# Kernel tuning notes

Hardware: AMD Instinct MI355X
Metric: run time of the kernel (lower is better)

The kernel has to match this reference:

```python
import jax, jax.numpy as jnp
import numpy as np

N = 100000
E = 800000
IN_DIM = 256
HEADS = 8
OUT_DIM = 32
OUT_ALL = HEADS * OUT_DIM  # 256 == IN_DIM -> residual is Identity
NEG_SLOPE = 0.2


def setup_inputs() -> dict:
    key = jax.random.key(0)
    ks = jax.random.split(key, 10)
    s_in = 1.0 / np.sqrt(IN_DIM)
    x = jax.random.normal(ks[0], (N, IN_DIM), dtype=jnp.float32)
    edge_index = jax.random.randint(ks[1], (2, E), 0, N, dtype=jnp.int64)
    Wl = jax.random.normal(ks[2], (IN_DIM, OUT_ALL), dtype=jnp.float32) * s_in
    bl = jnp.zeros((OUT_ALL,), dtype=jnp.float32)
    Wr = jax.random.normal(ks[3], (IN_DIM, OUT_ALL), dtype=jnp.float32) * s_in
    br = jnp.zeros((OUT_ALL,), dtype=jnp.float32)
    att = jax.random.normal(ks[4], (HEADS, OUT_DIM), dtype=jnp.float32) * (1.0 / np.sqrt(OUT_DIM))
    bias = jnp.zeros((OUT_ALL,), dtype=jnp.float32)
    gamma = jnp.ones((OUT_ALL,), dtype=jnp.float32)
    beta = jnp.zeros((OUT_ALL,), dtype=jnp.float32)
    return {"x": x, "edge_index": edge_index, "Wl": Wl, "bl": bl, "Wr": Wr,
            "br": br, "att": att, "bias": bias, "gamma": gamma, "beta": beta}


def reference(x, edge_index, Wl, bl, Wr, br, att, bias, gamma, beta):
    src, dst = edge_index[0], edge_index[1]
    # GATv2: separate transforms for source (lin_l) and target (lin_r)
    x_l = (x @ Wl + bl).reshape(N, HEADS, OUT_DIM)  # messages / source side
    x_r = (x @ Wr + br).reshape(N, HEADS, OUT_DIM)  # target side
    # edge-wise GATv2 score: a^T LeakyReLU(x_j + x_i)
    s = jax.nn.leaky_relu(x_l[src] + x_r[dst], NEG_SLOPE)  # [E, H, D]
    e = jnp.einsum('ehd,hd->eh', s, att)                   # [E, H]
    # segment softmax over incoming edges of each destination node
    m = jax.ops.segment_max(e, dst, num_segments=N)        # [N, H]
    p = jnp.exp(e - m[dst])                                # [E, H]
    denom = jax.ops.segment_sum(p, dst, num_segments=N)    # [N, H]
    denom = jnp.where(denom == 0, 1.0, denom)
    alpha = p / denom[dst]                                 # [E, H]
    # scatter-sum aggregate of alpha * lin_l(x_src)
    msg = alpha[:, :, None] * x_l[src]                     # [E, H, D]
    out = jax.ops.segment_sum(msg, dst, num_segments=N)    # [N, H, D]
    y = out.reshape(N, OUT_ALL) + bias
    # residual is Identity since in_dim == heads*out_dim
    z = y + x
    # LayerNorm then ELU
    mu = jnp.mean(z, axis=-1, keepdims=True)
    var = jnp.var(z, axis=-1, keepdims=True)
    zn = (z - mu) * jax.lax.rsqrt(var + 1e-5) * gamma + beta
    return jax.nn.elu(zn)
```

## Files before the change

### kernel.cpp

```cpp
#include <hip/hip_runtime.h>
#include <hip/hip_bf16.h>

#define NN 100000
#define EE 800000
#define DALL 256
#define NEG 0.2f

#define CNT_BLOCKS 3125
#define CVTW_BLOCKS 128
#define CVTX_BLOCKS 2048

typedef __attribute__((ext_vector_type(8))) short bf16x8;
typedef __attribute__((ext_vector_type(4))) float f32x4;

static __device__ __forceinline__ ushort f2b(float f) {
    __hip_bfloat16 h = __float2bfloat16(f);
    return *reinterpret_cast<ushort*>(&h);
}
static __device__ __forceinline__ float b2f(ushort u) {
    union { float f; unsigned v; } c; c.v = ((unsigned)u) << 16; return c.f;
}
static __device__ __forceinline__ void unpack8(uint4 u, float* v) {
    v[0] = b2f((ushort)(u.x & 0xffff)); v[1] = b2f((ushort)(u.x >> 16));
    v[2] = b2f((ushort)(u.y & 0xffff)); v[3] = b2f((ushort)(u.y >> 16));
    v[4] = b2f((ushort)(u.z & 0xffff)); v[5] = b2f((ushort)(u.z >> 16));
    v[6] = b2f((ushort)(u.w & 0xffff)); v[7] = b2f((ushort)(u.w >> 16));
}

__global__ __launch_bounds__(256) void fused_init(
    const float* __restrict__ x, const float* __restrict__ Wl,
    const float* __restrict__ Wr, const int* __restrict__ dst,
    ushort* __restrict__ xb, ushort* __restrict__ Wt, int* __restrict__ cnt)
{
    __shared__ float tile[32][33];
    int b = blockIdx.x;
    if (b < CNT_BLOCKS) {
        int e = b * 256 + threadIdx.x;
        if (e < EE) atomicAdd(&cnt[dst[e]], 1);
        return;
    }
    b -= CNT_BLOCKS;
    if (b < CVTW_BLOCKS) {
        int kt = (b & 7) * 32, nt = (b >> 3) * 32;
        int tx = threadIdx.x & 31, ty = threadIdx.x >> 5;
#pragma unroll
        for (int i = 0; i < 32; i += 8) {
            int k = kt + ty + i, n = nt + tx;
            float v = (n < 256) ? Wl[(size_t)k * 256 + n] : Wr[(size_t)k * 256 + (n - 256)];
            tile[ty + i][tx] = v;
        }
        __syncthreads();
#pragma unroll
        for (int i = 0; i < 32; i += 8) {
            int n = nt + ty + i, k = kt + tx;
            Wt[(size_t)n * 256 + k] = f2b(tile[tx][ty + i]);
        }
        return;
    }
    b -= CVTW_BLOCKS;
    const int total = NN * DALL / 8;
    for (int i = b * 256 + threadIdx.x; i < total; i += CVTX_BLOCKS * 256) {
        float4 a = reinterpret_cast<const float4*>(x)[i * 2];
        float4 c = reinterpret_cast<const float4*>(x)[i * 2 + 1];
        uint4 o;
        o.x = f2b(a.x) | ((unsigned)f2b(a.y) << 16);
        o.y = f2b(a.z) | ((unsigned)f2b(a.w) << 16);
        o.z = f2b(c.x) | ((unsigned)f2b(c.y) << 16);
        o.w = f2b(c.z) | ((unsigned)f2b(c.w) << 16);
        reinterpret_cast<uint4*>(xb)[i] = o;
    }
}

__global__ __launch_bounds__(512) void gemm_dual(
    const ushort* __restrict__ xb,
    const ushort* __restrict__ Wt,
    const float* __restrict__ bl, const float* __restrict__ br,
    ushort* __restrict__ xl, ushort* __restrict__ xr)
{
    __shared__ __align__(16) ushort smemA[2][128 * 32];
    __shared__ __align__(16) ushort smemB[2][256 * 32];

    const int bx = blockIdx.x;
    const int rowBase = (bx >> 1) * 128;
    const int colBase = (bx & 1) * 256;
    const int t = threadIdx.x, lane = t & 63, wave = t >> 6;
    const int wr = (wave >> 2) * 64;
    const int wc = (wave & 3) * 64;

    f32x4 acc[4][4];
#pragma unroll
    for (int m = 0; m < 4; ++m)
#pragma unroll
        for (int n = 0; n < 4; ++n) acc[m][n] = (f32x4){0.f, 0.f, 0.f, 0.f};

    auto STAGE = [&](int buf, int kb) {
        {
            int rc = t >> 2, slot = t & 3;
            int ga = rowBase + rc; if (ga >= NN) ga = NN - 1;
            const ushort* gp = xb + (size_t)ga * 256 + kb + slot * 8;
            ushort* lp = &smemA[buf][wave * 512];
            __builtin_amdgcn_global_load_lds(
                (const __attribute__((address_space(1))) unsigned int*)gp,
                (__attribute__((address_space(3))) unsigned int*)lp, 16, 0, 0);
        }
#pragma unroll
        for (int i = 0; i < 2; ++i) {
            int c = i * 512 + t;
            int rc = c >> 2, slot = c & 3;
            const ushort* gp = Wt + (size_t)(colBase + rc) * 256 + kb + slot * 8;
            ushort* lp = &smemB[buf][(i * 512 + wave * 64) * 8];
            __builtin_amdgcn_global_load_lds(
                (const __attribute__((address_space(1))) unsigned int*)gp,
                (__attribute__((address_space(3))) unsigned int*)lp, 16, 0, 0);
        }
    };

    STAGE(0, 0);
    __syncthreads();

#pragma unroll
    for (int s = 0; s < 8; ++s) {
        if (s < 7) STAGE((s + 1) & 1, (s + 1) * 32);
        const ushort* A = smemA[s & 1];
        const ushort* B = smemB[s & 1];
        bf16x8 af[4], bfr[4];
#pragma unroll
        for (int m = 0; m < 4; ++m)
            af[m] = *reinterpret_cast<const bf16x8*>(
                &A[(wr + m * 16 + (lane & 15)) * 32 + (lane >> 4) * 8]);
#pragma unroll
        for (int n = 0; n < 4; ++n)
            bfr[n] = *reinterpret_cast<const bf16x8*>(
                &B[(wc + n * 16 + (lane & 15)) * 32 + (lane >> 4) * 8]);
#pragma unroll
        for (int m = 0; m < 4; ++m)
#pragma unroll
            for (int n = 0; n < 4; ++n)
                acc[m][n] = __builtin_amdgcn_mfma_f32_16x16x32_bf16(
                    af[m], bfr[n], acc[m][n], 0, 0, 0);
        if (s < 7) __syncthreads();
    }

    const bool isL = (colBase == 0);
    ushort* OutP = isL ? xl : xr;
    const float* bvp = isL ? bl : br;

    int colLoc[4]; float bb[4];
#pragma unroll
    for (int n = 0; n < 4; ++n) {
        colLoc[n] = wc + n * 16 + (lane & 15);
        bb[n] = bvp[colLoc[n]];
    }
#pragma unroll
    for (int m = 0; m < 4; ++m) {
        int r0 = rowBase + wr + m * 16 + (lane >> 4) * 4;
#pragma unroll
        for (int r = 0; r < 4; ++r) {
            int row = r0 + r;
            if (row < NN) {
#pragma unroll
                for (int n = 0; n < 4; ++n)
                    OutP[(size_t)row * 256 + colLoc[n]] = f2b(acc[m][n][r] + bb[n]);
            }
        }
    }
}

__global__ __launch_bounds__(256) void scan_part1(const int* __restrict__ cnt,
                                                  int* __restrict__ bsums)
{
    __shared__ int red[256];
    int base = blockIdx.x * 1024 + threadIdx.x * 4;
    int s = 0;
#pragma unroll
    for (int k = 0; k < 4; ++k) { int i = base + k; if (i < NN) s += cnt[i]; }
    red[threadIdx.x] = s; __syncthreads();
    for (int off = 128; off > 0; off >>= 1) {
        if (threadIdx.x < off) red[threadIdx.x] += red[threadIdx.x + off];
        __syncthreads();
    }
    if (threadIdx.x == 0) bsums[blockIdx.x] = red[0];
}

__global__ __launch_bounds__(256) void scan_rowptr(const int* __restrict__ cnt,
                                                   const int* __restrict__ bsums,
                                                   int* __restrict__ rowptr)
{
    __shared__ int redB[256];
    __shared__ int pre[256];
    int tb = threadIdx.x;
    redB[tb] = (tb < (int)blockIdx.x) ? bsums[tb] : 0;
    __syncthreads();
    for (int off = 128; off > 0; off >>= 1) {
        if (tb < off) redB[tb] += redB[tb + off];
        __syncthreads();
    }
    int base0 = redB[0];

    int base = blockIdx.x * 1024 + tb * 4;
    int v[4]; int s = 0;
#pragma unroll
    for (int k = 0; k < 4; ++k) { int i = base + k; v[k] = (i < NN) ? cnt[i] : 0; s += v[k]; }
    pre[tb] = s; __syncthreads();
    for (int off = 1; off < 256; off <<= 1) {
        int tv = (tb >= off) ? pre[tb - off] : 0;
        __syncthreads();
        pre[tb] += tv;
        __syncthreads();
    }
    int excl = pre[tb] - s + base0;
#pragma unroll
    for (int k = 0; k < 4; ++k) {
        int i = base + k;
        if (i < NN) { rowptr[i] = excl; excl += v[k]; }
    }
}

__global__ __launch_bounds__(256) void fill_csr(const int* __restrict__ src,
                                                const int* __restrict__ dst,
                                                int* __restrict__ rowptr,
                                                int* __restrict__ srcs)
{
    int e = blockIdx.x * 256 + threadIdx.x;
    if (e >= EE) return;
    int pos = atomicAdd(&rowptr[dst[e]], 1);
    srcs[pos] = src[e];
}

__global__ __launch_bounds__(256) void aggregate_finalize(
    const ushort* __restrict__ xl, const ushort* __restrict__ xr,
    const int* __restrict__ srcs, const int* __restrict__ rowptr,
    const float* __restrict__ att, const ushort* __restrict__ xb,
    const float* __restrict__ bias, const float* __restrict__ gamma,
    const float* __restrict__ beta, float* __restrict__ out)
{
    int node = blockIdx.x * 4 + (threadIdx.x >> 6);
    if (node >= NN) return;
    int lane = threadIdx.x & 63;
    int half = lane >> 5;
    int dl = lane & 31;
    const int off = dl * 8;

    uint4 xru = *reinterpret_cast<const uint4*>(xr + (size_t)node * DALL + off);
    float xrv[8]; unpack8(xru, xrv);
    float atv[8];
    {
        float4 a0 = *reinterpret_cast<const float4*>(att + off);
        float4 a1 = *reinterpret_cast<const float4*>(att + off + 4);
        atv[0]=a0.x; atv[1]=a0.y; atv[2]=a0.z; atv[3]=a0.w;
        atv[4]=a1.x; atv[5]=a1.y; atv[6]=a1.z; atv[7]=a1.w;
    }

    int beg = node ? rowptr[node - 1] : 0;
    int end = rowptr[node];
    float a[8] = {0.f,0.f,0.f,0.f,0.f,0.f,0.f,0.f};
    float dsum = 0.f;

    for (int base = beg; base < end; base += 4) {
        int jA = base + half;
        int jB = base + 2 + half;
        bool vA = jA < end, vB = jB < end;
        int sA = srcs[vA ? jA : beg];
        int sB = srcs[vB ? jB : beg];
        uint4 gA = *reinterpret_cast<const uint4*>(xl + (size_t)sA * DALL + off);
        uint4 gB = *reinterpret_cast<const uint4*>(xl + (size_t)sB * DALL + off);
        float vAv[8], vBv[8]; unpack8(gA, vAv); unpack8(gB, vBv);
        float pA = 0.f, pB = 0.f;
#pragma unroll
        for (int i = 0; i < 8; ++i) {
            float z = vAv[i] + xrv[i];  pA += fmaxf(z, NEG * z) * atv[i];
            float z2 = vBv[i] + xrv[i]; pB += fmaxf(z2, NEG * z2) * atv[i];
        }
        pA += __shfl_xor(pA, 1); pA += __shfl_xor(pA, 2);
        pB += __shfl_xor(pB, 1); pB += __shfl_xor(pB, 2);
        float peA = vA ? __expf(pA) : 0.f;
        float peB = vB ? __expf(pB) : 0.f;
#pragma unroll
        for (int i = 0; i < 8; ++i) a[i] += peA * vAv[i] + peB * vBv[i];
        dsum += peA + peB;
    }

#pragma unroll
    for (int i = 0; i < 8; ++i) a[i] += __shfl_xor(a[i], 32);
    dsum += __shfl_xor(dsum, 32);
    float inv = dsum > 0.f ? 1.f / dsum : 0.f;

    uint4 xbu = *reinterpret_cast<const uint4*>(xb + (size_t)node * DALL + off);
    float xv[8]; unpack8(xbu, xv);
    float bvv[8], gvv[8], bev[8];
    {
        float4 b0 = *reinterpret_cast<const float4*>(bias + off);
        float4 b1 = *reinterpret_cast<const float4*>(bias + off + 4);
        bvv[0]=b0.x; bvv[1]=b0.y; bvv[2]=b0.z; bvv[3]=b0.w;
        bvv[4]=b1.x; bvv[5]=b1.y; bvv[6]=b1.z; bvv[7]=b1.w;
        float4 g0 = *reinterpret_cast<const float4*>(gamma + off);
        float4 g1 = *reinterpret_cast<const float4*>(gamma + off + 4);
        gvv[0]=g0.x; gvv[1]=g0.y; gvv[2]=g0.z; gvv[3]=g0.w;
        gvv[4]=g1.x; gvv[5]=g1.y; gvv[6]=g1.z; gvv[7]=g1.w;
        float4 e0 = *reinterpret_cast<const float4*>(beta + off);
        float4 e1 = *reinterpret_cast<const float4*>(beta + off + 4);
        bev[0]=e0.x; bev[1]=e0.y; bev[2]=e0.z; bev[3]=e0.w;
        bev[4]=e1.x; bev[5]=e1.y; bev[6]=e1.z; bev[7]=e1.w;
    }

    float y[8]; float sum = 0.f, sq = 0.f;
#pragma unroll
    for (int i = 0; i < 8; ++i) {
        y[i] = a[i] * inv + bvv[i] + xv[i];
        sum += y[i]; sq += y[i] * y[i];
    }
#pragma unroll
    for (int m = 1; m < 32; m <<= 1) {
        sum += __shfl_xor(sum, m);
        sq  += __shfl_xor(sq, m);
    }
    float mu  = sum * (1.0f / 256.0f);
    float var = sq * (1.0f / 256.0f) - mu * mu;
    float rr  = rsqrtf(var + 1e-5f);

    if (half == 0) {
        float4 o0, o1;
        float z0 = (y[0]-mu)*rr*gvv[0] + bev[0];
        float z1 = (y[1]-mu)*rr*gvv[1] + bev[1];
        float z2 = (y[2]-mu)*rr*gvv[2] + bev[2];
        float z3 = (y[3]-mu)*rr*gvv[3] + bev[3];
        float z4 = (y[4]-mu)*rr*gvv[4] + bev[4];
        float z5 = (y[5]-mu)*rr*gvv[5] + bev[5];
        float z6 = (y[6]-mu)*rr*gvv[6] + bev[6];
        float z7 = (y[7]-mu)*rr*gvv[7] + bev[7];
        o0.x = z0 > 0.f ? z0 : expm1f(z0);
        o0.y = z1 > 0.f ? z1 : expm1f(z1);
        o0.z = z2 > 0.f ? z2 : expm1f(z2);
        o0.w = z3 > 0.f ? z3 : expm1f(z3);
        o1.x = z4 > 0.f ? z4 : expm1f(z4);
        o1.y = z5 > 0.f ? z5 : expm1f(z5);
        o1.z = z6 > 0.f ? z6 : expm1f(z6);
        o1.w = z7 > 0.f ? z7 : expm1f(z7);
        *reinterpret_cast<float4*>(out + (size_t)node * DALL + off)     = o0;
        *reinterpret_cast<float4*>(out + (size_t)node * DALL + off + 4) = o1;
    }
}

extern "C" void kernel_launch(void* const* d_in, const int* in_sizes, int n_in,
                              void* d_out, int out_size, void* d_ws, size_t ws_size,
                              hipStream_t stream)
{
    const float* x    = (const float*)d_in[0];
    const int*   edge = (const int*)d_in[1];
    const float* Wl   = (const float*)d_in[2];
    const float* bl   = (const float*)d_in[3];
    const float* Wr   = (const float*)d_in[4];
    const float* br   = (const float*)d_in[5];
    const float* att  = (const float*)d_in[6];
    const float* bias = (const float*)d_in[7];
    const float* gamma= (const float*)d_in[8];
    const float* beta = (const float*)d_in[9];
    float* out = (float*)d_out;

    const int* srcIdx = edge;
    const int* dstIdx = edge + EE;

    ushort* xl = (ushort*)d_ws;
    ushort* xr = xl + (size_t)NN * DALL;
    ushort* xb = xr + (size_t)NN * DALL;
    ushort* Wt = xb + (size_t)NN * DALL;
    int* rowptr = (int*)(Wt + 512 * 256);
    int* cnt    = rowptr + NN + 1;
    int* srcs   = cnt + NN;
    int* bsums  = srcs + EE;

    const int SCAN_NB = (NN + 1023) / 1024;

    hipMemsetAsync(cnt, 0, NN * sizeof(int), stream);
    fused_init<<<CNT_BLOCKS + CVTW_BLOCKS + CVTX_BLOCKS, 256, 0, stream>>>(
        x, Wl, Wr, dstIdx, xb, Wt, cnt);
    gemm_dual<<<782 * 2, 512, 0, stream>>>(xb, Wt, bl, br, xl, xr);
    scan_part1<<<SCAN_NB, 256, 0, stream>>>(cnt, bsums);
    scan_rowptr<<<SCAN_NB, 256, 0, stream>>>(cnt, bsums, rowptr);
    fill_csr<<<(EE + 255) / 256, 256, 0, stream>>>(srcIdx, dstIdx, rowptr, srcs);
    aggregate_finalize<<<NN / 4, 256, 0, stream>>>(
        xl, xr, srcs, rowptr, att, xb, bias, gamma, beta, out);
}
```

Before: 280.3 us.

## Compute both Wl and Wr halves per GEMM block and use nontemporal streaming loads

The dual GEMM now has each 128-row block compute all 512 output columns (both lin_l and lin_r), so each x tile is loaded once instead of twice. Each wave holds a 64x128 accumulator tile, which doubles register use and LDS for B and may lower occupancy. Separately, streaming reads of x, xr and xb and the final output store use nontemporal load/store builtins to reduce cache pollution.

Result: no change. 280.7 us (+0.2%).

```diff
diff --git a/kernel.cpp b/kernel.cpp
--- a/kernel.cpp
+++ b/kernel.cpp
@@ -12,6 +12,7 @@
 
 typedef __attribute__((ext_vector_type(8))) short bf16x8;
 typedef __attribute__((ext_vector_type(4))) float f32x4;
+typedef __attribute__((ext_vector_type(4))) unsigned int u32x4;
 
 static __device__ __forceinline__ ushort f2b(float f) {
     __hip_bfloat16 h = __float2bfloat16(f);
@@ -25,6 +26,12 @@
     v[2] = b2f((ushort)(u.y & 0xffff)); v[3] = b2f((ushort)(u.y >> 16));
     v[4] = b2f((ushort)(u.z & 0xffff)); v[5] = b2f((ushort)(u.z >> 16));
     v[6] = b2f((ushort)(u.w & 0xffff)); v[7] = b2f((ushort)(u.w >> 16));
+}
+static __device__ __forceinline__ void unpack8v(u32x4 u, float* v) {
+    v[0] = b2f((ushort)(u[0] & 0xffff)); v[1] = b2f((ushort)(u[0] >> 16));
+    v[2] = b2f((ushort)(u[1] & 0xffff)); v[3] = b2f((ushort)(u[1] >> 16));
+    v[4] = b2f((ushort)(u[2] & 0xffff)); v[5] = b2f((ushort)(u[2] >> 16));
+    v[6] = b2f((ushort)(u[3] & 0xffff)); v[7] = b2f((ushort)(u[3] >> 16));
 }
 
 __global__ __launch_bounds__(256) void fused_init(
@@ -60,13 +67,13 @@
     b -= CVTW_BLOCKS;
     const int total = NN * DALL / 8;
     for (int i = b * 256 + threadIdx.x; i < total; i += CVTX_BLOCKS * 256) {
-        float4 a = reinterpret_cast<const float4*>(x)[i * 2];
-        float4 c = reinterpret_cast<const float4*>(x)[i * 2 + 1];
+        f32x4 a = __builtin_nontemporal_load(reinterpret_cast<const f32x4*>(x) + i * 2);
+        f32x4 c = __builtin_nontemporal_load(reinterpret_cast<const f32x4*>(x) + i * 2 + 1);
         uint4 o;
-        o.x = f2b(a.x) | ((unsigned)f2b(a.y) << 16);
-        o.y = f2b(a.z) | ((unsigned)f2b(a.w) << 16);
-        o.z = f2b(c.x) | ((unsigned)f2b(c.y) << 16);
-        o.w = f2b(c.z) | ((unsigned)f2b(c.w) << 16);
+        o.x = f2b(a[0]) | ((unsigned)f2b(a[1]) << 16);
+        o.y = f2b(a[2]) | ((unsigned)f2b(a[3]) << 16);
+        o.z = f2b(c[0]) | ((unsigned)f2b(c[1]) << 16);
+        o.w = f2b(c[2]) | ((unsigned)f2b(c[3]) << 16);
         reinterpret_cast<uint4*>(xb)[i] = o;
     }
 }
@@ -78,20 +85,18 @@
     ushort* __restrict__ xl, ushort* __restrict__ xr)
 {
     __shared__ __align__(16) ushort smemA[2][128 * 32];
-    __shared__ __align__(16) ushort smemB[2][256 * 32];
-
-    const int bx = blockIdx.x;
-    const int rowBase = (bx >> 1) * 128;
-    const int colBase = (bx & 1) * 256;
+    __shared__ __align__(16) ushort smemB[2][512 * 32];
+
+    const int rowBase = blockIdx.x * 128;
     const int t = threadIdx.x, lane = t & 63, wave = t >> 6;
-    const int wr = (wave >> 2) * 64;
-    const int wc = (wave & 3) * 64;
-
-    f32x4 acc[4][4];
+    const int wr  = (wave >> 2) * 64;
+    const int wcg = (wave & 3) * 128;
+
+    f32x4 acc[4][8];
 #pragma unroll
     for (int m = 0; m < 4; ++m)
 #pragma unroll
-        for (int n = 0; n < 4; ++n) acc[m][n] = (f32x4){0.f, 0.f, 0.f, 0.f};
+        for (int n = 0; n < 8; ++n) acc[m][n] = (f32x4){0.f, 0.f, 0.f, 0.f};
 
     auto STAGE = [&](int buf, int kb) {
         {
@@ -104,10 +109,10 @@
                 (__attribute__((address_space(3))) unsigned int*)lp, 16, 0, 0);
         }
 #pragma unroll
-        for (int i = 0; i < 2; ++i) {
+        for (int i = 0; i < 4; ++i) {
             int c = i * 512 + t;
             int rc = c >> 2, slot = c & 3;
-            const ushort* gp = Wt + (size_t)(colBase + rc) * 256 + kb + slot * 8;
+            const ushort* gp = Wt + (size_t)rc * 256 + kb + slot * 8;
             ushort* lp = &smemB[buf][(i * 512 + wave * 64) * 8];
             __builtin_amdgcn_global_load_lds(
                 (const __attribute__((address_space(1))) unsigned int*)gp,
@@ -123,32 +128,33 @@
         if (s < 7) STAGE((s + 1) & 1, (s + 1) * 32);
         const ushort* A = smemA[s & 1];
         const ushort* B = smemB[s & 1];
-        bf16x8 af[4], bfr[4];
+        bf16x8 af[4], bfr[8];
 #pragma unroll
         for (int m = 0; m < 4; ++m)
             af[m] = *reinterpret_cast<const bf16x8*>(
                 &A[(wr + m * 16 + (lane & 15)) * 32 + (lane >> 4) * 8]);
 #pragma unroll
-        for (int n = 0; n < 4; ++n)
+        for (int n = 0; n < 8; ++n)
             bfr[n] = *reinterpret_cast<const bf16x8*>(
-                &B[(wc + n * 16 + (lane & 15)) * 32 + (lane >> 4) * 8]);
+                &B[(wcg + n * 16 + (lane & 15)) * 32 + (lane >> 4) * 8]);
 #pragma unroll
         for (int m = 0; m < 4; ++m)
 #pragma unroll
-            for (int n = 0; n < 4; ++n)
+            for (int n = 0; n < 8; ++n)
                 acc[m][n] = __builtin_amdgcn_mfma_f32_16x16x32_bf16(
                     af[m], bfr[n], acc[m][n], 0, 0, 0);
         if (s < 7) __syncthreads();
     }
 
-    const bool isL = (colBase == 0);
+    const bool isL = (wcg < 256);
     ushort* OutP = isL ? xl : xr;
     const float* bvp = isL ? bl : br;
-
-    int colLoc[4]; float bb[4];
-#pragma unroll
-    for (int n = 0; n < 4; ++n) {
-        colLoc[n] = wc + n * 16 + (lane & 15);
+    const int cb0 = wcg & 255;
+
+    int colLoc[8]; float bb[8];
+#pragma unroll
+    for (int n = 0; n < 8; ++n) {
+        colLoc[n] = cb0 + n * 16 + (lane & 15);
         bb[n] = bvp[colLoc[n]];
     }
 #pragma unroll
@@ -159,7 +165,7 @@
             int row = r0 + r;
             if (row < NN) {
 #pragma unroll
-                for (int n = 0; n < 4; ++n)
+                for (int n = 0; n < 8; ++n)
                     OutP[(size_t)row * 256 + colLoc[n]] = f2b(acc[m][n][r] + bb[n]);
             }
         }
@@ -241,8 +247,9 @@
     int dl = lane & 31;
     const int off = dl * 8;
 
-    uint4 xru = *reinterpret_cast<const uint4*>(xr + (size_t)node * DALL + off);
-    float xrv[8]; unpack8(xru, xrv);
+    u32x4 xru = __builtin_nontemporal_load(
+        reinterpret_cast<const u32x4*>(xr + (size_t)node * DALL + off));
+    float xrv[8]; unpack8v(xru, xrv);
     float atv[8];
     {
         float4 a0 = *reinterpret_cast<const float4*>(att + off);
@@ -285,8 +292,9 @@
     dsum += __shfl_xor(dsum, 32);
     float inv = dsum > 0.f ? 1.f / dsum : 0.f;
 
-    uint4 xbu = *reinterpret_cast<const uint4*>(xb + (size_t)node * DALL + off);
-    float xv[8]; unpack8(xbu, xv);
+    u32x4 xbu = __builtin_nontemporal_load(
+        reinterpret_cast<const u32x4*>(xb + (size_t)node * DALL + off));
+    float xv[8]; unpack8v(xbu, xv);
     float bvv[8], gvv[8], bev[8];
     {
         float4 b0 = *reinterpret_cast<const float4*>(bias + off);
@@ -319,7 +327,7 @@
     float rr  = rsqrtf(var + 1e-5f);
 
     if (half == 0) {
-        float4 o0, o1;
+        f32x4 o0, o1;
         float z0 = (y[0]-mu)*rr*gvv[0] + bev[0];
         float z1 = (y[1]-mu)*rr*gvv[1] + bev[1];
         float z2 = (y[2]-mu)*rr*gvv[2] + bev[2];
@@ -328,16 +336,18 @@
         float z5 = (y[5]-mu)*rr*gvv[5] + bev[5];
         float z6 = (y[6]-mu)*rr*gvv[6] + bev[6];
         float z7 = (y[7]-mu)*rr*gvv[7] + bev[7];
-        o0.x = z0 > 0.f ? z0 : expm1f(z0);
-        o0.y = z1 > 0.f ? z1 : expm1f(z1);
-        o0.z = z2 > 0.f ? z2 : expm1f(z2);
-        o0.w = z3 > 0.f ? z3 : expm1f(z3);
-        o1.x = z4 > 0.f ? z4 : expm1f(z4);
-        o1.y = z5 > 0.f ? z5 : expm1f(z5);
-        o1.z = z6 > 0.f ? z6 : expm1f(z6);
-        o1.w = z7 > 0.f ? z7 : expm1f(z7);
-        *reinterpret_cast<float4*>(out + (size_t)node * DALL + off)     = o0;
-        *reinterpret_cast<float4*>(out + (size_t)node * DALL + off + 4) = o1;
+        o0[0] = z0 > 0.f ? z0 : expm1f(z0);
+        o0[1] = z1 > 0.f ? z1 : expm1f(z1);
+        o0[2] = z2 > 0.f ? z2 : expm1f(z2);
+        o0[3] = z3 > 0.f ? z3 : expm1f(z3);
+        o1[0] = z4 > 0.f ? z4 : expm1f(z4);
+        o1[1] = z5 > 0.f ? z5 : expm1f(z5);
+        o1[2] = z6 > 0.f ? z6 : expm1f(z6);
+        o1[3] = z7 > 0.f ? z7 : expm1f(z7);
+        __builtin_nontemporal_store(o0,
+            reinterpret_cast<f32x4*>(out + (size_t)node * DALL + off));
+        __builtin_nontemporal_store(o1,
+            reinterpret_cast<f32x4*>(out + (size_t)node * DALL + off + 4));
     }
 }
 
@@ -374,7 +384,7 @@
     hipMemsetAsync(cnt, 0, NN * sizeof(int), stream);
     fused_init<<<CNT_BLOCKS + CVTW_BLOCKS + CVTX_BLOCKS, 256, 0, stream>>>(
         x, Wl, Wr, dstIdx, xb, Wt, cnt);
-    gemm_dual<<<782 * 2, 512, 0, stream>>>(xb, Wt, bl, br, xl, xr);
+    gemm_dual<<<(NN + 127) / 128, 512, 0, stream>>>(xb, Wt, bl, br, xl, xr);
     scan_part1<<<SCAN_NB, 256, 0, stream>>>(cnt, bsums);
     scan_rowptr<<<SCAN_NB, 256, 0, stream>>>(cnt, bsums, rowptr);
     fill_csr<<<(EE + 255) / 256, 256, 0, stream>>>(srcIdx, dstIdx, rowptr, srcs);
```
